# Optimization experiments

Hardware: AMD Instinct MI355X
Metric: run time of the kernel (lower is better)

The kernel has to match this reference:

```python
import jax, jax.numpy as jnp
import numpy as np

B, N, D = 2, 2048, 1024
H = 16
HD = D // H  # 64
ROPE_BASE = 10000.0


def setup_inputs() -> dict:
    key = jax.random.key(0)
    ks = jax.random.split(key, 5)
    s = 0.02
    return {
        "x": jax.random.normal(ks[0], (B, N, D), dtype=jnp.float32),
        "qkv_w": jax.random.normal(ks[1], (3 * D, D), dtype=jnp.float32) * s,
        "qkv_b": jax.random.normal(ks[2], (3 * D,), dtype=jnp.float32) * s,
        "proj_w": jax.random.normal(ks[3], (D, D), dtype=jnp.float32) * s,
        "proj_b": jax.random.normal(ks[4], (D,), dtype=jnp.float32) * s,
    }


def _rotate_half(t):
    # interleaved pairs: (x1,x2) -> (-x2,x1), matching lucidrains RotaryEmbedding
    t = t.reshape(*t.shape[:-1], -1, 2)
    x1, x2 = t[..., 0], t[..., 1]
    return jnp.stack((-x2, x1), axis=-1).reshape(*t.shape[:-2], -1)


def _apply_rope(t, cos, sin):
    # t: [B, H, N, HD]; cos/sin: [N, HD]
    return t * cos + _rotate_half(t) * sin


def reference(x, qkv_w, qkv_b, proj_w, proj_b):
    b, n, d = x.shape
    scale = HD ** -0.5

    qkv = x @ qkv_w.T + qkv_b                      # [B, N, 3D]
    qkv = qkv.reshape(b, n, 3, H, HD)
    qkv = jnp.transpose(qkv, (2, 0, 3, 1, 4))       # [3, B, H, N, HD]
    q, k, v = qkv[0], qkv[1], qkv[2]

    # RoPE (lang freqs, interpolate_factor=1)
    inv_freq = 1.0 / (ROPE_BASE ** (jnp.arange(0, HD, 2, dtype=jnp.float32) / HD))
    freqs = jnp.arange(n, dtype=jnp.float32)[:, None] * inv_freq[None, :]  # [N, HD/2]
    freqs = jnp.repeat(freqs, 2, axis=-1)           # [N, HD] interleaved
    cos, sin = jnp.cos(freqs), jnp.sin(freqs)
    q = _apply_rope(q, cos, sin)
    k = _apply_rope(k, cos, sin)

    scores = jnp.einsum('bhid,bhjd->bhij', q, k) * scale  # [B, H, N, N]
    causal = jnp.triu(jnp.ones((n, n), dtype=bool), k=1)
    scores = jnp.where(causal, -jnp.inf, scores)
    attn = jax.nn.softmax(scores, axis=-1)

    out = jnp.einsum('bhij,bhjd->bhid', attn, v)    # [B, H, N, HD]
    out = jnp.transpose(out, (0, 2, 1, 3)).reshape(b, n, d)
    return out @ proj_w.T + proj_b
```

## Files before the change

### kernel.cpp

```cpp
#include <hip/hip_runtime.h>
#include <hip/hip_bf16.h>
#include <cstdint>
#include <cstddef>

typedef __hip_bfloat16 bf16;
typedef short bf16x8 __attribute__((ext_vector_type(8)));
typedef float f32x4 __attribute__((ext_vector_type(4)));
typedef int i32x4 __attribute__((ext_vector_type(4)));

#define MFMA16(a, b, c) __builtin_amdgcn_mfma_f32_16x16x32_bf16((a), (b), (c), 0, 0, 0)

__device__ __forceinline__ void glds16(const bf16* g, bf16* l)
{
    __builtin_amdgcn_global_load_lds(
        (const __attribute__((address_space(1))) void*)g,
        (__attribute__((address_space(3))) void*)l, 16, 0, 0);
}

__global__ void cvt_f32_bf16(const float* __restrict__ in, bf16* __restrict__ out, int n4)
{
    int i = blockIdx.x * blockDim.x + threadIdx.x;
    if (i >= n4) return;
    float4 v = *reinterpret_cast<const float4*>(in + (size_t)i * 4);
    __align__(8) bf16 tmp[4];
    tmp[0] = __float2bfloat16(v.x);
    tmp[1] = __float2bfloat16(v.y);
    tmp[2] = __float2bfloat16(v.z);
    tmp[3] = __float2bfloat16(v.w);
    *reinterpret_cast<short4*>(out + (size_t)i * 4) = *reinterpret_cast<short4*>(tmp);
}

__global__ void rope_table_kernel(float2* __restrict__ tab)
{
    int i = blockIdx.x * blockDim.x + threadIdx.x;
    int pos = i >> 5, f = i & 31;
    float inv = powf(10000.f, -(float)f * (1.f / 32.f));
    float ang = (float)pos * inv;
    tab[i] = make_float2(cosf(ang), sinf(ang));
}

__global__ void rope_apply_kernel(bf16* __restrict__ qkv, const float2* __restrict__ tab)
{
    int idx = blockIdx.x * blockDim.x + threadIdx.x;
    int row = idx >> 8;
    int cc  = (idx & 255) * 8;
    int pos = row & 2047;
    int hd  = cc & 63;
    bf16* p = qkv + (size_t)row * 3072 + cc;
    i32x4 v = *reinterpret_cast<const i32x4*>(p);
    bf16* e = reinterpret_cast<bf16*>(&v);
    const float2* tb = tab + pos * 32 + (hd >> 1);
#pragma unroll
    for (int pp = 0; pp < 4; ++pp) {
        float2 cs = tb[pp];
        float x1 = __bfloat162float(e[2 * pp]);
        float x2 = __bfloat162float(e[2 * pp + 1]);
        e[2 * pp]     = __float2bfloat16(x1 * cs.x - x2 * cs.y);
        e[2 * pp + 1] = __float2bfloat16(x2 * cs.x + x1 * cs.y);
    }
    *reinterpret_cast<i32x4*>(p) = v;
}

__device__ inline void store_out(float* p, float v) { *p = v; }
__device__ inline void store_out(bf16* p, float v) { *p = __float2bfloat16(v); }

template <typename OutT>
__global__ void gemm_bt_kernel(const bf16* __restrict__ A, const bf16* __restrict__ BT,
                               const float* __restrict__ bias, OutT* __restrict__ C,
                               int M, int N, int K)
{
    constexpr int BM = 128, BN = 128, BK = 32;
    __shared__ __align__(16) bf16 Al[BM * BK];
    __shared__ __align__(16) bf16 Bl[BN * BK];

    const int tid = threadIdx.x;
    const int l = tid & 63;
    const int w = tid >> 6;
    const int wr = w >> 1, wc = w & 1;
    const int l15 = l & 15, lhi = l >> 4;
    const int row0 = blockIdx.x * BM, col0 = blockIdx.y * BN;

    const int ar0 = tid >> 2, ar1 = (tid + 256) >> 2;
    const int ac  = (tid & 3) * 8;
    const bf16* Ag0 = A + (size_t)(row0 + ar0) * K + ac;
    const bf16* Ag1 = A + (size_t)(row0 + ar1) * K + ac;
    const bf16* Bg0 = BT + (size_t)(col0 + ar0) * K + ac;
    const bf16* Bg1 = BT + (size_t)(col0 + ar1) * K + ac;
    const int wbase = (tid & 192) * 8;
    bf16* sA0 = &Al[wbase];
    bf16* sA1 = &Al[2048 + wbase];
    bf16* sB0 = &Bl[wbase];
    bf16* sB1 = &Bl[2048 + wbase];

    f32x4 acc[4][4] = {};

    for (int k0 = 0; k0 < K; k0 += BK) {
        __syncthreads();
        glds16(Ag0 + k0, sA0);
        glds16(Ag1 + k0, sA1);
        glds16(Bg0 + k0, sB0);
        glds16(Bg1 + k0, sB1);
        __syncthreads();
        bf16x8 af[4], bfr[4];
#pragma unroll
        for (int m = 0; m < 4; ++m)
            af[m] = *reinterpret_cast<const bf16x8*>(&Al[(wr * 64 + m * 16 + l15) * BK + lhi * 8]);
#pragma unroll
        for (int n = 0; n < 4; ++n)
            bfr[n] = *reinterpret_cast<const bf16x8*>(&Bl[(wc * 64 + n * 16 + l15) * BK + lhi * 8]);
#pragma unroll
        for (int m = 0; m < 4; ++m)
#pragma unroll
            for (int n = 0; n < 4; ++n)
                acc[m][n] = MFMA16(af[m], bfr[n], acc[m][n]);
    }

#pragma unroll
    for (int m = 0; m < 4; ++m) {
#pragma unroll
        for (int n = 0; n < 4; ++n) {
            int col = col0 + wc * 64 + n * 16 + l15;
            float bs = bias[col];
#pragma unroll
            for (int j = 0; j < 4; ++j) {
                int row = row0 + wr * 64 + m * 16 + lhi * 4 + j;
                store_out(&C[(size_t)row * N + col], acc[m][n][j] + bs);
            }
        }
    }
}

__global__ void attn_kernel(const bf16* __restrict__ qkv, bf16* __restrict__ outp)
{
    constexpr int LDK = 72;
    __shared__ __align__(16) bf16 Kl[2][64 * LDK];
    __shared__ __align__(16) bf16 Vt[2][64 * LDK];
    __shared__ __align__(16) bf16 Pl[64 * LDK];

    const int bh = blockIdx.x;
    const int b = bh >> 4, h = bh & 15;
    const int q0 = (31 - blockIdx.y) * 64;
    const int tid = threadIdx.x;
    const int w = tid >> 6, l = tid & 63;
    const int l15 = l & 15, lhi = l >> 4;

    const size_t RS = 3072;
    const bf16* base = qkv + (size_t)b * 2048 * RS;

    bf16x8 qf0, qf1;
    {
        const bf16* qr = base + (size_t)(q0 + w * 16 + l15) * RS + h * 64 + lhi * 8;
        qf0 = *reinterpret_cast<const bf16x8*>(qr);
        qf1 = *reinterpret_cast<const bf16x8*>(qr + 32);
    }

    const int kr  = tid >> 3;
    const int kc8 = (tid & 7) * 8;
    const bf16* kp = base + (size_t)kr * RS + 1024 + h * 64 + kc8;
    const bf16* vp = base + (size_t)(w * 16) * RS + 2048 + h * 64 + l;

    i32x4 ka, kb;
    __align__(16) bf16 vt16[16];

    ka = *reinterpret_cast<const i32x4*>(kp);
    kb = *reinterpret_cast<const i32x4*>(kp + 32 * RS);
#pragma unroll
    for (int j = 0; j < 16; ++j) vt16[j] = vp[(size_t)j * RS];
    *reinterpret_cast<i32x4*>(&Kl[0][kr * LDK + kc8])        = ka;
    *reinterpret_cast<i32x4*>(&Kl[0][(kr + 32) * LDK + kc8]) = kb;
    *reinterpret_cast<i32x4*>(&Vt[0][l * LDK + w * 16])      = *reinterpret_cast<const i32x4*>(&vt16[0]);
    *reinterpret_cast<i32x4*>(&Vt[0][l * LDK + w * 16 + 8])  = *reinterpret_cast<const i32x4*>(&vt16[8]);
    __syncthreads();

    float m_run[4], l_run[4];
    f32x4 o_acc[4] = {};
#pragma unroll
    for (int j = 0; j < 4; ++j) { m_run[j] = -1e30f; l_run[j] = 0.f; }

    const int ntiles = q0 / 64 + 1;
    int cur = 0;
    for (int t = 0; t < ntiles; ++t) {
        const int kv0 = t * 64;
        const bool pf = (t + 1 < ntiles);
        if (pf) {
            kp += 64 * RS;
            vp += 64 * RS;
            ka = *reinterpret_cast<const i32x4*>(kp);
            kb = *reinterpret_cast<const i32x4*>(kp + 32 * RS);
#pragma unroll
            for (int j = 0; j < 16; ++j) vt16[j] = vp[(size_t)j * RS];
        }

        const bf16* Kc = &Kl[cur][0];
        const bf16* Vc = &Vt[cur][0];

        f32x4 s[4] = {};
#pragma unroll
        for (int n = 0; n < 4; ++n) {
            bf16x8 kf0 = *reinterpret_cast<const bf16x8*>(&Kc[(n * 16 + l15) * LDK + lhi * 8]);
            bf16x8 kf1 = *reinterpret_cast<const bf16x8*>(&Kc[(n * 16 + l15) * LDK + 32 + lhi * 8]);
            s[n] = MFMA16(qf0, kf0, s[n]);
            s[n] = MFMA16(qf1, kf1, s[n]);
        }

        const int qrow = q0 + w * 16 + lhi * 4;
#pragma unroll
        for (int n = 0; n < 4; ++n) {
            const int kvc = kv0 + n * 16 + l15;
#pragma unroll
            for (int j = 0; j < 4; ++j) {
                float v = s[n][j] * 0.125f;
                s[n][j] = (kvc > qrow + j) ? -1e30f : v;
            }
        }

        float alpha[4];
#pragma unroll
        for (int j = 0; j < 4; ++j) {
            float rm = fmaxf(fmaxf(s[0][j], s[1][j]), fmaxf(s[2][j], s[3][j]));
            rm = fmaxf(rm, __shfl_xor(rm, 1));
            rm = fmaxf(rm, __shfl_xor(rm, 2));
            rm = fmaxf(rm, __shfl_xor(rm, 4));
            rm = fmaxf(rm, __shfl_xor(rm, 8));
            float mnew = fmaxf(m_run[j], rm);
            alpha[j] = __expf(m_run[j] - mnew);
            m_run[j] = mnew;
        }
        float rs[4] = {0.f, 0.f, 0.f, 0.f};
#pragma unroll
        for (int n = 0; n < 4; ++n)
#pragma unroll
            for (int j = 0; j < 4; ++j) {
                float p = __expf(s[n][j] - m_run[j]);
                s[n][j] = p;
                rs[j] += p;
            }
#pragma unroll
        for (int j = 0; j < 4; ++j) {
            float r = rs[j];
            r += __shfl_xor(r, 1);
            r += __shfl_xor(r, 2);
            r += __shfl_xor(r, 4);
            r += __shfl_xor(r, 8);
            l_run[j] = l_run[j] * alpha[j] + r;
            o_acc[0][j] *= alpha[j];
            o_acc[1][j] *= alpha[j];
            o_acc[2][j] *= alpha[j];
            o_acc[3][j] *= alpha[j];
        }

        bf16* Pw = &Pl[w * 16 * LDK];
#pragma unroll
        for (int n = 0; n < 4; ++n)
#pragma unroll
            for (int j = 0; j < 4; ++j)
                Pw[(lhi * 4 + j) * LDK + n * 16 + l15] = __float2bfloat16(s[n][j]);

        bf16x8 pa0 = *reinterpret_cast<const bf16x8*>(&Pw[l15 * LDK + lhi * 8]);
        bf16x8 pa1 = *reinterpret_cast<const bf16x8*>(&Pw[l15 * LDK + 32 + lhi * 8]);
#pragma unroll
        for (int t2 = 0; t2 < 4; ++t2) {
            bf16x8 vf0 = *reinterpret_cast<const bf16x8*>(&Vc[(t2 * 16 + l15) * LDK + lhi * 8]);
            bf16x8 vf1 = *reinterpret_cast<const bf16x8*>(&Vc[(t2 * 16 + l15) * LDK + 32 + lhi * 8]);
            o_acc[t2] = MFMA16(pa0, vf0, o_acc[t2]);
            o_acc[t2] = MFMA16(pa1, vf1, o_acc[t2]);
        }

        if (pf) {
            const int nxt = cur ^ 1;
            *reinterpret_cast<i32x4*>(&Kl[nxt][kr * LDK + kc8])        = ka;
            *reinterpret_cast<i32x4*>(&Kl[nxt][(kr + 32) * LDK + kc8]) = kb;
            *reinterpret_cast<i32x4*>(&Vt[nxt][l * LDK + w * 16])      = *reinterpret_cast<const i32x4*>(&vt16[0]);
            *reinterpret_cast<i32x4*>(&Vt[nxt][l * LDK + w * 16 + 8])  = *reinterpret_cast<const i32x4*>(&vt16[8]);
            __syncthreads();
            cur = nxt;
        }
    }

#pragma unroll
    for (int j = 0; j < 4; ++j) {
        float inv = 1.f / l_run[j];
        size_t row = (size_t)(b * 2048 + q0 + w * 16 + lhi * 4 + j);
#pragma unroll
        for (int t2 = 0; t2 < 4; ++t2)
            outp[row * 1024 + h * 64 + t2 * 16 + l15] = __float2bfloat16(o_acc[t2][j] * inv);
    }
}

extern "C" void kernel_launch(void* const* d_in, const int* in_sizes, int n_in,
                              void* d_out, int out_size, void* d_ws, size_t ws_size,
                              hipStream_t stream)
{
    const float* x      = (const float*)d_in[0];
    const float* qkv_w  = (const float*)d_in[1];
    const float* qkv_b  = (const float*)d_in[2];
    const float* proj_w = (const float*)d_in[3];
    const float* proj_b = (const float*)d_in[4];
    float* out = (float*)d_out;

    char* ws = (char*)d_ws;
    bf16* x_bf   = (bf16*)ws;  ws += (size_t)4096 * 1024 * 2;
    bf16* wq_bf  = (bf16*)ws;  ws += (size_t)3072 * 1024 * 2;
    bf16* wp_bf  = (bf16*)ws;  ws += (size_t)1024 * 1024 * 2;
    bf16* qkvbuf = (bf16*)ws;  ws += (size_t)4096 * 3072 * 2;
    bf16* aout   = (bf16*)ws;  ws += (size_t)4096 * 1024 * 2;
    float2* tab  = (float2*)ws;

    cvt_f32_bf16<<<4096, 256, 0, stream>>>(x, x_bf, 1048576);
    cvt_f32_bf16<<<3072, 256, 0, stream>>>(qkv_w, wq_bf, 786432);
    cvt_f32_bf16<<<1024, 256, 0, stream>>>(proj_w, wp_bf, 262144);
    rope_table_kernel<<<256, 256, 0, stream>>>(tab);

    gemm_bt_kernel<bf16><<<dim3(32, 24), 256, 0, stream>>>(x_bf, wq_bf, qkv_b, qkvbuf, 4096, 3072, 1024);
    rope_apply_kernel<<<4096, 256, 0, stream>>>(qkvbuf, tab);
    attn_kernel<<<dim3(32, 32), 256, 0, stream>>>(qkvbuf, aout);
    gemm_bt_kernel<float><<<dim3(32, 8), 256, 0, stream>>>(aout, wp_bf, proj_b, out, 4096, 1024, 1024);
}
```

Baseline: 218.6 us.

## Rewrite attention with 32x32 MFMA, 128-row query blocks, and register-resident P

The attention kernel now processes 128 query rows per block, with 32 rows per wave, using 32x32x16 bf16 MFMA. It computes S^T = K·Q so the probabilities stay in registers and are exchanged across half-waves by shuffles, which removes the P round-trip through shared memory. Q is prescaled by log2(e)/8 so exp2f can be used, and the rescale of the running output is skipped while the max grows by no more than 8 (lazy rescaling). It also skips fully masked tiles per wave and adds launch bounds. The costs are more register pressure, a coarser grid, and the extra bf16 rounding of Q after prescaling.

```diff
diff --git a/kernel.cpp b/kernel.cpp
--- a/kernel.cpp
+++ b/kernel.cpp
@@ -6,15 +6,25 @@
 typedef __hip_bfloat16 bf16;
 typedef short bf16x8 __attribute__((ext_vector_type(8)));
 typedef float f32x4 __attribute__((ext_vector_type(4)));
+typedef float f32x16 __attribute__((ext_vector_type(16)));
 typedef int i32x4 __attribute__((ext_vector_type(4)));
 
 #define MFMA16(a, b, c) __builtin_amdgcn_mfma_f32_16x16x32_bf16((a), (b), (c), 0, 0, 0)
+#define MFMA32(a, b, c) __builtin_amdgcn_mfma_f32_32x32x16_bf16((a), (b), (c), 0, 0, 0)
 
 __device__ __forceinline__ void glds16(const bf16* g, bf16* l)
 {
     __builtin_amdgcn_global_load_lds(
         (const __attribute__((address_space(1))) void*)g,
         (__attribute__((address_space(3))) void*)l, 16, 0, 0);
+}
+
+__device__ __forceinline__ unsigned pkbf16(float a, float b)
+{
+    bf16 ba = __float2bfloat16(a), bb = __float2bfloat16(b);
+    unsigned ua = *reinterpret_cast<unsigned short*>(&ba);
+    unsigned ub = *reinterpret_cast<unsigned short*>(&bb);
+    return ua | (ub << 16);
 }
 
 __global__ void cvt_f32_bf16(const float* __restrict__ in, bf16* __restrict__ out, int n4)
@@ -130,28 +140,38 @@
     }
 }
 
-__global__ void attn_kernel(const bf16* __restrict__ qkv, bf16* __restrict__ outp)
-{
-    constexpr int LDK = 72;
+__global__ __launch_bounds__(256, 2)
+void attn_kernel(const bf16* __restrict__ qkv, bf16* __restrict__ outp)
+{
+    constexpr int LDK = 68, LDV = 68;
     __shared__ __align__(16) bf16 Kl[2][64 * LDK];
-    __shared__ __align__(16) bf16 Vt[2][64 * LDK];
-    __shared__ __align__(16) bf16 Pl[64 * LDK];
+    __shared__ __align__(16) bf16 Vt[2][64 * LDV];
+    __shared__ float wred[4][32];
 
     const int bh = blockIdx.x;
     const int b = bh >> 4, h = bh & 15;
-    const int q0 = (31 - blockIdx.y) * 64;
+    const int q0b = (15 - (int)blockIdx.y) * 128;
     const int tid = threadIdx.x;
     const int w = tid >> 6, l = tid & 63;
-    const int l15 = l & 15, lhi = l >> 4;
+    const int q31 = l & 31, hi = l >> 5;
+    const int q0w = q0b + w * 32;
+    const int qa = q0w + q31;
 
     const size_t RS = 3072;
     const bf16* base = qkv + (size_t)b * 2048 * RS;
 
-    bf16x8 qf0, qf1;
+    bf16x8 qf[4];
     {
-        const bf16* qr = base + (size_t)(q0 + w * 16 + l15) * RS + h * 64 + lhi * 8;
-        qf0 = *reinterpret_cast<const bf16x8*>(qr);
-        qf1 = *reinterpret_cast<const bf16x8*>(qr + 32);
+        const bf16* qr = base + (size_t)qa * RS + h * 64 + hi * 8;
+#pragma unroll
+        for (int s = 0; s < 4; ++s) {
+            bf16x8 v = *reinterpret_cast<const bf16x8*>(qr + s * 16);
+            bf16* e = reinterpret_cast<bf16*>(&v);
+#pragma unroll
+            for (int j = 0; j < 8; ++j)
+                e[j] = __float2bfloat16(__bfloat162float(e[j]) * 0.18033688f);
+            qf[s] = v;
+        }
     }
 
     const int kr  = tid >> 3;
@@ -168,16 +188,14 @@
     for (int j = 0; j < 16; ++j) vt16[j] = vp[(size_t)j * RS];
     *reinterpret_cast<i32x4*>(&Kl[0][kr * LDK + kc8])        = ka;
     *reinterpret_cast<i32x4*>(&Kl[0][(kr + 32) * LDK + kc8]) = kb;
-    *reinterpret_cast<i32x4*>(&Vt[0][l * LDK + w * 16])      = *reinterpret_cast<const i32x4*>(&vt16[0]);
-    *reinterpret_cast<i32x4*>(&Vt[0][l * LDK + w * 16 + 8])  = *reinterpret_cast<const i32x4*>(&vt16[8]);
+    *reinterpret_cast<i32x4*>(&Vt[0][l * LDV + w * 16])      = *reinterpret_cast<const i32x4*>(&vt16[0]);
+    *reinterpret_cast<i32x4*>(&Vt[0][l * LDV + w * 16 + 8])  = *reinterpret_cast<const i32x4*>(&vt16[8]);
     __syncthreads();
 
-    float m_run[4], l_run[4];
-    f32x4 o_acc[4] = {};
-#pragma unroll
-    for (int j = 0; j < 4; ++j) { m_run[j] = -1e30f; l_run[j] = 0.f; }
-
-    const int ntiles = q0 / 64 + 1;
+    float m_run = -1e30f, l_run = 0.f;
+    f32x16 o0 = {}, o1 = {};
+
+    const int ntiles = q0b / 64 + 2;
     int cur = 0;
     for (int t = 0; t < ntiles; ++t) {
         const int kv0 = t * 64;
@@ -191,99 +209,109 @@
             for (int j = 0; j < 16; ++j) vt16[j] = vp[(size_t)j * RS];
         }
 
-        const bf16* Kc = &Kl[cur][0];
-        const bf16* Vc = &Vt[cur][0];
-
-        f32x4 s[4] = {};
-#pragma unroll
-        for (int n = 0; n < 4; ++n) {
-            bf16x8 kf0 = *reinterpret_cast<const bf16x8*>(&Kc[(n * 16 + l15) * LDK + lhi * 8]);
-            bf16x8 kf1 = *reinterpret_cast<const bf16x8*>(&Kc[(n * 16 + l15) * LDK + 32 + lhi * 8]);
-            s[n] = MFMA16(qf0, kf0, s[n]);
-            s[n] = MFMA16(qf1, kf1, s[n]);
-        }
-
-        const int qrow = q0 + w * 16 + lhi * 4;
-#pragma unroll
-        for (int n = 0; n < 4; ++n) {
-            const int kvc = kv0 + n * 16 + l15;
-#pragma unroll
-            for (int j = 0; j < 4; ++j) {
-                float v = s[n][j] * 0.125f;
-                s[n][j] = (kvc > qrow + j) ? -1e30f : v;
-            }
-        }
-
-        float alpha[4];
-#pragma unroll
-        for (int j = 0; j < 4; ++j) {
-            float rm = fmaxf(fmaxf(s[0][j], s[1][j]), fmaxf(s[2][j], s[3][j]));
-            rm = fmaxf(rm, __shfl_xor(rm, 1));
-            rm = fmaxf(rm, __shfl_xor(rm, 2));
-            rm = fmaxf(rm, __shfl_xor(rm, 4));
-            rm = fmaxf(rm, __shfl_xor(rm, 8));
-            float mnew = fmaxf(m_run[j], rm);
-            alpha[j] = __expf(m_run[j] - mnew);
-            m_run[j] = mnew;
-        }
-        float rs[4] = {0.f, 0.f, 0.f, 0.f};
-#pragma unroll
-        for (int n = 0; n < 4; ++n)
-#pragma unroll
-            for (int j = 0; j < 4; ++j) {
-                float p = __expf(s[n][j] - m_run[j]);
-                s[n][j] = p;
-                rs[j] += p;
-            }
-#pragma unroll
-        for (int j = 0; j < 4; ++j) {
-            float r = rs[j];
-            r += __shfl_xor(r, 1);
-            r += __shfl_xor(r, 2);
-            r += __shfl_xor(r, 4);
-            r += __shfl_xor(r, 8);
-            l_run[j] = l_run[j] * alpha[j] + r;
-            o_acc[0][j] *= alpha[j];
-            o_acc[1][j] *= alpha[j];
-            o_acc[2][j] *= alpha[j];
-            o_acc[3][j] *= alpha[j];
-        }
-
-        bf16* Pw = &Pl[w * 16 * LDK];
-#pragma unroll
-        for (int n = 0; n < 4; ++n)
-#pragma unroll
-            for (int j = 0; j < 4; ++j)
-                Pw[(lhi * 4 + j) * LDK + n * 16 + l15] = __float2bfloat16(s[n][j]);
-
-        bf16x8 pa0 = *reinterpret_cast<const bf16x8*>(&Pw[l15 * LDK + lhi * 8]);
-        bf16x8 pa1 = *reinterpret_cast<const bf16x8*>(&Pw[l15 * LDK + 32 + lhi * 8]);
-#pragma unroll
-        for (int t2 = 0; t2 < 4; ++t2) {
-            bf16x8 vf0 = *reinterpret_cast<const bf16x8*>(&Vc[(t2 * 16 + l15) * LDK + lhi * 8]);
-            bf16x8 vf1 = *reinterpret_cast<const bf16x8*>(&Vc[(t2 * 16 + l15) * LDK + 32 + lhi * 8]);
-            o_acc[t2] = MFMA16(pa0, vf0, o_acc[t2]);
-            o_acc[t2] = MFMA16(pa1, vf1, o_acc[t2]);
+        if (kv0 <= q0w + 31) {
+            const bf16* Kc = &Kl[cur][0];
+            const bf16* Vc = &Vt[cur][0];
+
+            f32x16 p0 = {}, p1 = {};
+#pragma unroll
+            for (int s = 0; s < 4; ++s) {
+                bf16x8 kf0 = *reinterpret_cast<const bf16x8*>(&Kc[q31 * LDK + s * 16 + hi * 8]);
+                bf16x8 kf1 = *reinterpret_cast<const bf16x8*>(&Kc[(32 + q31) * LDK + s * 16 + hi * 8]);
+                p0 = MFMA32(kf0, qf[s], p0);
+                p1 = MFMA32(kf1, qf[s], p1);
+            }
+
+            if (kv0 + 63 > q0w) {
+                const int lim = qa - kv0 - 4 * hi;
+#pragma unroll
+                for (int r = 0; r < 16; ++r) {
+                    const int cr = (r & 3) + 8 * (r >> 2);
+                    if (cr > lim)      p0[r] = -1e30f;
+                    if (cr + 32 > lim) p1[r] = -1e30f;
+                }
+            }
+
+            float rm = p0[0];
+#pragma unroll
+            for (int r = 1; r < 16; ++r) rm = fmaxf(rm, p0[r]);
+#pragma unroll
+            for (int r = 0; r < 16; ++r) rm = fmaxf(rm, p1[r]);
+            rm = fmaxf(rm, __shfl_xor(rm, 32));
+
+            if (!__all(rm - m_run <= 8.0f)) {
+                float mnew = fmaxf(m_run, rm);
+                float alpha = exp2f(m_run - mnew);
+                m_run = mnew;
+                l_run *= alpha;
+                if (hi == 0) wred[w][q31] = alpha;
+#pragma unroll
+                for (int g = 0; g < 4; ++g) {
+                    f32x4 av = *reinterpret_cast<const f32x4*>(&wred[w][8 * g + 4 * hi]);
+#pragma unroll
+                    for (int tt = 0; tt < 4; ++tt) {
+                        o0[4 * g + tt] *= av[tt];
+                        o1[4 * g + tt] *= av[tt];
+                    }
+                }
+            }
+
+            float rsum = 0.f;
+#pragma unroll
+            for (int r = 0; r < 16; ++r) { p0[r] = exp2f(p0[r] - m_run); rsum += p0[r]; }
+#pragma unroll
+            for (int r = 0; r < 16; ++r) { p1[r] = exp2f(p1[r] - m_run); rsum += p1[r]; }
+            rsum += __shfl_xor(rsum, 32);
+            l_run += rsum;
+
+            unsigned A[8], Bv[8];
+#pragma unroll
+            for (int m = 0; m < 4; ++m) {
+                A[m]      = pkbf16(p0[4 * m],     p0[4 * m + 1]);
+                Bv[m]     = pkbf16(p0[4 * m + 2], p0[4 * m + 3]);
+                A[m + 4]  = pkbf16(p1[4 * m],     p1[4 * m + 1]);
+                Bv[m + 4] = pkbf16(p1[4 * m + 2], p1[4 * m + 3]);
+            }
+
+#pragma unroll
+            for (int ks = 0; ks < 4; ++ks) {
+                unsigned sa = hi ? A[2 * ks]  : A[2 * ks + 1];
+                unsigned sb = hi ? Bv[2 * ks] : Bv[2 * ks + 1];
+                unsigned ra = (unsigned)__shfl_xor((int)sa, 32);
+                unsigned rb = (unsigned)__shfl_xor((int)sb, 32);
+                union { unsigned u[4]; bf16x8 v; } pa;
+                if (hi == 0) { pa.u[0] = A[2 * ks];  pa.u[1] = Bv[2 * ks];  pa.u[2] = ra; pa.u[3] = rb; }
+                else         { pa.u[0] = ra; pa.u[1] = rb; pa.u[2] = A[2 * ks + 1]; pa.u[3] = Bv[2 * ks + 1]; }
+                bf16x8 vf0 = *reinterpret_cast<const bf16x8*>(&Vc[q31 * LDV + ks * 16 + hi * 8]);
+                bf16x8 vf1 = *reinterpret_cast<const bf16x8*>(&Vc[(32 + q31) * LDV + ks * 16 + hi * 8]);
+                o0 = MFMA32(pa.v, vf0, o0);
+                o1 = MFMA32(pa.v, vf1, o1);
+            }
         }
 
         if (pf) {
             const int nxt = cur ^ 1;
             *reinterpret_cast<i32x4*>(&Kl[nxt][kr * LDK + kc8])        = ka;
             *reinterpret_cast<i32x4*>(&Kl[nxt][(kr + 32) * LDK + kc8]) = kb;
-            *reinterpret_cast<i32x4*>(&Vt[nxt][l * LDK + w * 16])      = *reinterpret_cast<const i32x4*>(&vt16[0]);
-            *reinterpret_cast<i32x4*>(&Vt[nxt][l * LDK + w * 16 + 8])  = *reinterpret_cast<const i32x4*>(&vt16[8]);
+            *reinterpret_cast<i32x4*>(&Vt[nxt][l * LDV + w * 16])      = *reinterpret_cast<const i32x4*>(&vt16[0]);
+            *reinterpret_cast<i32x4*>(&Vt[nxt][l * LDV + w * 16 + 8])  = *reinterpret_cast<const i32x4*>(&vt16[8]);
             __syncthreads();
             cur = nxt;
         }
     }
 
-#pragma unroll
-    for (int j = 0; j < 4; ++j) {
-        float inv = 1.f / l_run[j];
-        size_t row = (size_t)(b * 2048 + q0 + w * 16 + lhi * 4 + j);
-#pragma unroll
-        for (int t2 = 0; t2 < 4; ++t2)
-            outp[row * 1024 + h * 64 + t2 * 16 + l15] = __float2bfloat16(o_acc[t2][j] * inv);
+    if (hi == 0) wred[w][q31] = 1.0f / l_run;
+#pragma unroll
+    for (int g = 0; g < 4; ++g) {
+        f32x4 iv = *reinterpret_cast<const f32x4*>(&wred[w][8 * g + 4 * hi]);
+#pragma unroll
+        for (int tt = 0; tt < 4; ++tt) {
+            const int r = 4 * g + tt;
+            const int qrow = q0w + 8 * g + 4 * hi + tt;
+            bf16* op = outp + (size_t)(b * 2048 + qrow) * 1024 + h * 64 + q31;
+            op[0]  = __float2bfloat16(o0[r] * iv[tt]);
+            op[32] = __float2bfloat16(o1[r] * iv[tt]);
+        }
     }
 }
 
@@ -313,6 +341,6 @@
 
     gemm_bt_kernel<bf16><<<dim3(32, 24), 256, 0, stream>>>(x_bf, wq_bf, qkv_b, qkvbuf, 4096, 3072, 1024);
     rope_apply_kernel<<<4096, 256, 0, stream>>>(qkvbuf, tab);
-    attn_kernel<<<dim3(32, 32), 256, 0, stream>>>(qkvbuf, aout);
+    attn_kernel<<<dim3(32, 16), 256, 0, stream>>>(qkvbuf, aout);
     gemm_bt_kernel<float><<<dim3(32, 8), 256, 0, stream>>>(aout, wp_bf, proj_b, out, 4096, 1024, 1024);
 }
```

New measurement: 271.7 us. 24.3% more time.
